# Optimization experiments

Measured on AMD Instinct MI355X. Metric: run time of the kernel, lower is better.

## Reference

```python
import jax, jax.numpy as jnp
import numpy as np

SCALE = 1.0 / 16.0      # spatial scale: image coords -> feature-map coords (stride-16 backbone)
OUT = 7                 # roi_pool_outsize
RATIO = 2               # sampling_ratio
NUM_CLASSES = 21
HID = 1024
SCORE_THRESH = 0.05
NMS_THRESH = 0.5
DET = 100               # detections_per_img
MIN_SIZE = 0.01
LOG_MAX = float(np.log(1000.0 / 16.0))  # standard bbox decode dw/dh clamp


def _bilinear(feat, ys, xs):
    # feat [C,H,W]; ys [Py], xs [Px] -> [C,Py,Px] (torchvision roi_align interpolation, aligned=False)
    C, H, W = feat.shape
    vy = (ys > -1.0) & (ys < H)
    vx = (xs > -1.0) & (xs < W)
    y = jnp.clip(ys, 0.0, H - 1.0)
    x = jnp.clip(xs, 0.0, W - 1.0)
    y0 = jnp.floor(y).astype(jnp.int32)
    x0 = jnp.floor(x).astype(jnp.int32)
    y1 = jnp.minimum(y0 + 1, H - 1)
    x1 = jnp.minimum(x0 + 1, W - 1)
    ly = (y - y0)[:, None]
    lx = (x - x0)[None, :]
    f00 = feat[:, y0[:, None], x0[None, :]]
    f01 = feat[:, y0[:, None], x1[None, :]]
    f10 = feat[:, y1[:, None], x0[None, :]]
    f11 = feat[:, y1[:, None], x1[None, :]]
    val = (f00 * (1.0 - ly) * (1.0 - lx) + f01 * (1.0 - ly) * lx
           + f10 * ly * (1.0 - lx) + f11 * ly * lx)
    return val * (vy[:, None] & vx[None, :])


def _roi_align(features, boxes, bidx):
    # features [N,C,H,W], boxes [R,4] (image coords), bidx [R] -> [R,C,OUT,OUT]
    N, C, H, W = features.shape
    b = boxes * SCALE
    rw = jnp.maximum(b[:, 2] - b[:, 0], 1.0)
    rh = jnp.maximum(b[:, 3] - b[:, 1], 1.0)
    bw = rw / OUT
    bh = rh / OUT
    # per-bin sample offsets: (ph + (i+0.5)/ratio) for ph in [0,OUT), i in [0,RATIO)
    g = (jnp.arange(OUT, dtype=jnp.float32)[:, None]
         + (jnp.arange(RATIO, dtype=jnp.float32)[None, :] + 0.5) / RATIO).reshape(-1)  # [OUT*RATIO]
    ys = b[:, 1][:, None] + g[None, :] * bh[:, None]  # [R, OUT*RATIO]
    xs = b[:, 0][:, None] + g[None, :] * bw[:, None]
    vals = jax.vmap(lambda i, yr, xr: _bilinear(features[i], yr, xr))(bidx, ys, xs)  # [R,C,P,P]
    R = boxes.shape[0]
    return vals.reshape(R, C, OUT, RATIO, OUT, RATIO).mean(axis=(3, 5))


def _decode(deltas, props):
    # deltas [R,K,4], props [R,4]; weights (10,10,5,5) as in the module
    pw = props[:, 2] - props[:, 0]
    ph = props[:, 3] - props[:, 1]
    pcx = props[:, 0] + 0.5 * pw
    pcy = props[:, 1] + 0.5 * ph
    dx = deltas[..., 0] / 10.0
    dy = deltas[..., 1] / 10.0
    dw = jnp.minimum(deltas[..., 2] / 5.0, LOG_MAX)
    dh = jnp.minimum(deltas[..., 3] / 5.0, LOG_MAX)
    cx = dx * pw[:, None] + pcx[:, None]
    cy = dy * ph[:, None] + pcy[:, None]
    w = jnp.exp(dw) * pw[:, None]
    h = jnp.exp(dh) * ph[:, None]
    return jnp.stack([cx - 0.5 * w, cy - 0.5 * h, cx + 0.5 * w, cy + 0.5 * h], axis=-1)


def _per_image(scores, boxes, img):
    # scores [S,K], boxes [S,K,4]. Drop background class, flatten, filter, class-aware NMS, top-DET.
    S, K = scores.shape
    sc = scores[:, 1:].reshape(-1)                 # [M]
    bx = boxes[:, 1:, :].reshape(-1, 4)            # [M,4]
    lb = jnp.broadcast_to(jnp.arange(1, K, dtype=jnp.int32)[None, :], (S, K - 1)).reshape(-1)
    wv = bx[:, 2] - bx[:, 0]
    hv = bx[:, 3] - bx[:, 1]
    valid = (sc > SCORE_THRESH) & (wv >= MIN_SIZE) & (hv >= MIN_SIZE)
    live0 = jnp.where(valid, sc, -1.0)
    # batched_nms via per-class coordinate offsets
    nb = bx + (lb.astype(bx.dtype) * (img + 1.0))[:, None]
    areas = (nb[:, 2] - nb[:, 0]) * (nb[:, 3] - nb[:, 1])

    def step(live, _):
        i = jnp.argmax(live)
        s = live[i]
        b = nb[i]
        xx1 = jnp.maximum(b[0], nb[:, 0])
        yy1 = jnp.maximum(b[1], nb[:, 1])
        xx2 = jnp.minimum(b[2], nb[:, 2])
        yy2 = jnp.minimum(b[3], nb[:, 3])
        inter = jnp.maximum(xx2 - xx1, 0.0) * jnp.maximum(yy2 - yy1, 0.0)
        area_i = (b[2] - b[0]) * (b[3] - b[1])
        iou = inter / (area_i + areas - inter + 1e-9)
        live = jnp.where(iou > NMS_THRESH, -1.0, live)  # also suppresses i itself (iou=1)
        return live, (i, s)

    _, (idxs, svals) = jax.lax.scan(step, live0, None, length=DET)
    keep = svals > SCORE_THRESH
    out_boxes = jnp.where(keep[:, None], bx[idxs], 0.0)
    out_scores = jnp.where(keep, svals, 0.0)
    out_labels = jnp.where(keep, lb[idxs], 0)
    return out_boxes, out_scores, out_labels


def _forward(features, proposals, w1, b1, w2, b2, wc, bc, wb, bb, image_size):
    N, C, H, W = features.shape
    S = proposals.shape[1]
    props = proposals.reshape(-1, 4)
    bidx = jnp.repeat(jnp.arange(N), S)
    feats = _roi_align(features, props, bidx)          # [R,C,7,7]
    x = feats.reshape(N * S, -1)                       # [R, C*49]
    h = jax.nn.relu(x @ w1 + b1)
    h = jax.nn.relu(h @ w2 + b2)
    cls = h @ wc + bc                                  # [R,K]
    deltas = (h @ wb + bb).reshape(N * S, NUM_CLASSES, 4)
    scores = jax.nn.softmax(cls, axis=-1)
    boxes = _decode(deltas, props)                     # [R,K,4]
    img = float(image_size)
    boxes = jnp.clip(boxes, 0.0, img)                  # square image -> clip both coords to [0,img]
    scores = scores.reshape(N, S, NUM_CLASSES)
    boxes = boxes.reshape(N, S, NUM_CLASSES, 4)
    return jax.vmap(lambda s, bx: _per_image(s, bx, img))(scores, boxes)


def setup_inputs() -> dict:
    key = jax.random.key(0)
    ks = jax.random.split(key, 12)
    N, S, C, H, W = 2, 512, 512, 50, 50
    IMG = 800
    features = jax.random.normal(ks[0], (N, C, H, W), jnp.float32)
    x1 = jax.random.uniform(ks[1], (N, S)) * (IMG - 80.0)
    y1 = jax.random.uniform(ks[2], (N, S)) * (IMG - 80.0)
    x2 = jnp.minimum(x1 + 16.0 + jax.random.uniform(ks[3], (N, S)) * 180.0, float(IMG))
    y2 = jnp.minimum(y1 + 16.0 + jax.random.uniform(ks[4], (N, S)) * 180.0, float(IMG))
    proposals = jnp.stack([x1, y1, x2, y2], axis=-1)
    D = C * OUT * OUT  # 25088
    w1 = jax.random.normal(ks[5], (D, HID), jnp.float32) * 0.01
    b1 = jnp.zeros((HID,), jnp.float32)
    w2 = jax.random.normal(ks[6], (HID, HID), jnp.float32) * 0.02
    b2 = jnp.zeros((HID,), jnp.float32)
    wc = jax.random.normal(ks[7], (HID, NUM_CLASSES), jnp.float32) * 0.05
    bc = jnp.zeros((NUM_CLASSES,), jnp.float32)
    wb = jax.random.normal(ks[8], (HID, NUM_CLASSES * 4), jnp.float32) * 0.02
    bb = jnp.zeros((NUM_CLASSES * 4,), jnp.float32)
    return {"features": features, "proposals": proposals, "w1": w1, "b1": b1,
            "w2": w2, "b2": b2, "wc": wc, "bc": bc, "wb": wb, "bb": bb,
            "image_size": IMG}


def reference(features, proposals, w1, b1, w2, b2, wc, bc, wb, bb, image_size):
    boxes, scores, labels = _forward(features, proposals, w1, b1, w2, b2, wc, bc, wb, bb, image_size)
    return boxes, scores, labels
```

## Files before the change

kernel.cpp:

```cpp
#include <hip/hip_runtime.h>
#include <cmath>

#define NIMG 2
#define SPROP 512
#define NROI 1024
#define CCH 512
#define FH 50
#define FW 50
#define K1 25088
#define HID 1024
#define NCLS 21
#define NDET 100
#define IMGSZ 800.0f
#define LOGMAX 4.135166556742356f
#define MCAND 10240
#define ZSPLIT 8
#define KCHUNK 3136
#define ZSPLIT2 4
#define KCHUNK2 256

typedef unsigned short u16;
typedef __attribute__((ext_vector_type(8))) short short8;
typedef __attribute__((ext_vector_type(4))) float f32x4;
typedef __attribute__((ext_vector_type(16))) float f32x16;

__device__ __forceinline__ u16 f2bf(float x) {
  unsigned int u = __float_as_uint(x);
  u += 0x7fffu + ((u >> 16) & 1u);
  return (u16)(u >> 16);
}
__device__ __forceinline__ float bf2f(u16 h) {
  return __uint_as_float(((unsigned int)h) << 16);
}

template <bool BF16OUT>
__global__ __launch_bounds__(256) void roi_kernel(
    const float* __restrict__ feat, const float* __restrict__ props,
    float* __restrict__ X, u16* __restrict__ Xhi, u16* __restrict__ Xlo) {
  const int r = blockIdx.x;
  const int n = r >> 9;
  const int tid = threadIdx.x;
  __shared__ float tile[32][256];
  __shared__ int sy0[14], sy1[14], sx0[14], sx1[14];
  __shared__ float sly[14], slx[14], svy[14], svx[14];

  const float p0 = props[r * 4 + 0] * 0.0625f;
  const float p1 = props[r * 4 + 1] * 0.0625f;
  const float p2 = props[r * 4 + 2] * 0.0625f;
  const float p3 = props[r * 4 + 3] * 0.0625f;
  const float bw = fmaxf(p2 - p0, 1.0f) / 7.0f;
  const float bh = fmaxf(p3 - p1, 1.0f) / 7.0f;

  if (tid < 14) {
    const int j = tid;
    const float g = (float)(j >> 1) + ((float)(j & 1) + 0.5f) * 0.5f;
    float y = p1 + g * bh;
    svy[j] = (y > -1.0f && y < (float)FH) ? 1.0f : 0.0f;
    float yc = fminf(fmaxf(y, 0.0f), (float)(FH - 1));
    int y0 = (int)floorf(yc);
    sy0[j] = y0; sy1[j] = min(y0 + 1, FH - 1); sly[j] = yc - (float)y0;
    float x = p0 + g * bw;
    svx[j] = (x > -1.0f && x < (float)FW) ? 1.0f : 0.0f;
    float xc = fminf(fmaxf(x, 0.0f), (float)(FW - 1));
    int x0 = (int)floorf(xc);
    sx0[j] = x0; sx1[j] = min(x0 + 1, FW - 1); slx[j] = xc - (float)x0;
  }
  __syncthreads();
  const int ymin = sy0[0], xmin = sx0[0];
  const float* fb = feat + (size_t)n * CCH * (FH * FW);

  for (int cc = 0; cc < 16; ++cc) {
    const int c0 = cc * 32;
#pragma unroll
    for (int e = 0; e < 32; ++e) {
      const int idx = tid + e * 256;
      const int c = idx >> 8, p = idx & 255;
      const int gy = min(ymin + (p >> 4), FH - 1);
      const int gx = min(xmin + (p & 15), FW - 1);
      tile[c][p] = fb[(size_t)(c0 + c) * (FH * FW) + gy * FW + gx];
    }
    __syncthreads();
#pragma unroll
    for (int e = 0; e < 7; ++e) {
      const int idx = tid + e * 256;
      if (idx < 1568) {
        const int c = idx / 49;
        const int s = idx - c * 49;
        const int oy = s / 7, ox = s - (s / 7) * 7;
        float acc = 0.0f;
#pragma unroll
        for (int sy = 0; sy < 2; ++sy) {
          const int yj = oy * 2 + sy;
          const int py0 = sy0[yj] - ymin, py1 = sy1[yj] - ymin;
          const float ly = sly[yj], vy = svy[yj];
#pragma unroll
          for (int sx = 0; sx < 2; ++sx) {
            const int xj = ox * 2 + sx;
            const int px0 = sx0[xj] - xmin, px1 = sx1[xj] - xmin;
            const float lx = slx[xj], vx = svx[xj];
            const float f00 = tile[c][py0 * 16 + px0];
            const float f01 = tile[c][py0 * 16 + px1];
            const float f10 = tile[c][py1 * 16 + px0];
            const float f11 = tile[c][py1 * 16 + px1];
            float v = f00 * (1.0f - ly) * (1.0f - lx) + f01 * (1.0f - ly) * lx +
                      f10 * ly * (1.0f - lx) + f11 * ly * lx;
            acc += v * (vy * vx);
          }
        }
        const float v = acc * 0.25f;
        const size_t k = (size_t)r * K1 + (size_t)(c0 + c) * 49 + s;
        if (BF16OUT) {
          const u16 h = f2bf(v);
          Xhi[k] = h;
          Xlo[k] = f2bf(v - bf2f(h));
        } else {
          X[k] = v;
        }
      }
    }
    __syncthreads();
  }
}

template <int KDIM>
__global__ __launch_bounds__(256) void convw_kernel(
    const float* __restrict__ w, u16* __restrict__ Wh, u16* __restrict__ Wl) {
  __shared__ u16 sh[64][65], sl[64][65];
  const int k0 = blockIdx.x * 64;
  const int n0 = blockIdx.y * 64;
  const int t = threadIdx.x;
#pragma unroll
  for (int e = 0; e < 16; ++e) {
    const int idx = t + e * 256;
    const int kl = idx >> 6, nl = idx & 63;
    const float v = w[(size_t)(k0 + kl) * HID + n0 + nl];
    const u16 h = f2bf(v);
    sh[kl][nl] = h;
    sl[kl][nl] = f2bf(v - bf2f(h));
  }
  __syncthreads();
#pragma unroll
  for (int e = 0; e < 16; ++e) {
    const int idx = t + e * 256;
    const int nl = idx >> 6, kl = idx & 63;
    Wh[(size_t)(n0 + nl) * KDIM + k0 + kl] = sh[kl][nl];
    Wl[(size_t)(n0 + nl) * KDIM + k0 + kl] = sl[kl][nl];
  }
}

template <int KS, int KCH>
__global__ __launch_bounds__(256, 2) void gemm_mfma_split(
    const u16* __restrict__ Ahg, const u16* __restrict__ Alg,
    const u16* __restrict__ Bhg, const u16* __restrict__ Blg,
    float* __restrict__ CP) {
  __shared__ u16 Ah[128][40], Al[128][40], Bh[128][40], Bl[128][40];
  const int tid = threadIdx.x;
  const int lane = tid & 63;
  const int wv = tid >> 6;
  const int wm = (wv >> 1) * 64;
  const int wn = (wv & 1) * 64;
  const int mT = blockIdx.y << 7;
  const int nT = blockIdx.x << 7;
  const int kz = blockIdx.z * KCH;

  const int r0 = tid >> 2, q0 = (tid & 3) << 3;
  const int r1 = r0 + 64;

  f32x16 acc[2][2];
#pragma unroll
  for (int i = 0; i < 2; ++i)
#pragma unroll
    for (int j = 0; j < 2; ++j)
#pragma unroll
      for (int e = 0; e < 16; ++e) acc[i][j][e] = 0.0f;

  const size_t a0off = (size_t)(mT + r0) * KS + q0;
  const size_t a1off = (size_t)(mT + r1) * KS + q0;
  const size_t b0off = (size_t)(nT + r0) * KS + q0;
  const size_t b1off = (size_t)(nT + r1) * KS + q0;

  const int fm = lane & 31;
  const int fq = (lane >> 5) << 3;

  uint4 va0 = *(const uint4*)(Ahg + a0off + kz);
  uint4 va1 = *(const uint4*)(Ahg + a1off + kz);
  uint4 vl0 = *(const uint4*)(Alg + a0off + kz);
  uint4 vl1 = *(const uint4*)(Alg + a1off + kz);
  uint4 vb0 = *(const uint4*)(Bhg + b0off + kz);
  uint4 vb1 = *(const uint4*)(Bhg + b1off + kz);
  uint4 vm0 = *(const uint4*)(Blg + b0off + kz);
  uint4 vm1 = *(const uint4*)(Blg + b1off + kz);

  for (int kb = kz; kb < kz + KCH; kb += 32) {
    *(uint4*)(&Ah[r0][q0]) = va0;
    *(uint4*)(&Ah[r1][q0]) = va1;
    *(uint4*)(&Al[r0][q0]) = vl0;
    *(uint4*)(&Al[r1][q0]) = vl1;
    *(uint4*)(&Bh[r0][q0]) = vb0;
    *(uint4*)(&Bh[r1][q0]) = vb1;
    *(uint4*)(&Bl[r0][q0]) = vm0;
    *(uint4*)(&Bl[r1][q0]) = vm1;
    __syncthreads();

    const int kn = kb + 32;
    if (kn < kz + KCH) {
      va0 = *(const uint4*)(Ahg + a0off + kn);
      va1 = *(const uint4*)(Ahg + a1off + kn);
      vl0 = *(const uint4*)(Alg + a0off + kn);
      vl1 = *(const uint4*)(Alg + a1off + kn);
      vb0 = *(const uint4*)(Bhg + b0off + kn);
      vb1 = *(const uint4*)(Bhg + b1off + kn);
      vm0 = *(const uint4*)(Blg + b0off + kn);
      vm1 = *(const uint4*)(Blg + b1off + kn);
    }

#pragma unroll
    for (int kh = 0; kh < 2; ++kh) {
      const int ko = kh * 16 + fq;
      short8 fah[2], fal[2], fbh[2], fbl[2];
#pragma unroll
      for (int t = 0; t < 2; ++t) {
        fah[t] = *(const short8*)(&Ah[wm + t * 32 + fm][ko]);
        fal[t] = *(const short8*)(&Al[wm + t * 32 + fm][ko]);
        fbh[t] = *(const short8*)(&Bh[wn + t * 32 + fm][ko]);
        fbl[t] = *(const short8*)(&Bl[wn + t * 32 + fm][ko]);
      }
#pragma unroll
      for (int ti = 0; ti < 2; ++ti)
#pragma unroll
        for (int tj = 0; tj < 2; ++tj) {
          acc[ti][tj] = __builtin_amdgcn_mfma_f32_32x32x16_bf16(
              fah[ti], fbh[tj], acc[ti][tj], 0, 0, 0);
          acc[ti][tj] = __builtin_amdgcn_mfma_f32_32x32x16_bf16(
              fah[ti], fbl[tj], acc[ti][tj], 0, 0, 0);
          acc[ti][tj] = __builtin_amdgcn_mfma_f32_32x32x16_bf16(
              fal[ti], fbh[tj], acc[ti][tj], 0, 0, 0);
        }
    }
    __syncthreads();
  }

  float* Cp = CP + (size_t)blockIdx.z * ((size_t)NROI * HID);
  const int ccol = nT + wn + (lane & 31);
  const int rbase = mT + wm + 4 * (lane >> 5);
#pragma unroll
  for (int ti = 0; ti < 2; ++ti)
#pragma unroll
    for (int tj = 0; tj < 2; ++tj)
#pragma unroll
      for (int rg = 0; rg < 16; ++rg) {
        const int row = rbase + ti * 32 + (rg & 3) + 8 * (rg >> 2);
        Cp[(size_t)row * HID + ccol + tj * 32] = acc[ti][tj][rg];
      }
}

__global__ __launch_bounds__(256) void gemm1_kernel(
    const float* __restrict__ A, const float* __restrict__ B,
    float* __restrict__ CP) {
  __shared__ float As[16][68];
  __shared__ float Bs[16][68];
  const int tid = threadIdx.x;
  const int mTile = blockIdx.y << 6;
  const int nTile = blockIdx.x << 6;
  const int k0 = blockIdx.z * KCHUNK;
  const int ty = tid >> 4, tx = tid & 15;
  const int ar = tid >> 2, ac = (tid & 3) << 2;
  const int br = tid >> 4, bcl = (tid & 15) << 2;
  float acc[4][4] = {};

  for (int kb = k0; kb < k0 + KCHUNK; kb += 16) {
    const float4 av = *(const float4*)(A + (size_t)(mTile + ar) * K1 + kb + ac);
    const float4 bv = *(const float4*)(B + (size_t)(kb + br) * HID + nTile + bcl);
    As[ac + 0][ar] = av.x; As[ac + 1][ar] = av.y;
    As[ac + 2][ar] = av.z; As[ac + 3][ar] = av.w;
    *(float4*)(&Bs[br][bcl]) = bv;
    __syncthreads();
#pragma unroll
    for (int kk = 0; kk < 16; ++kk) {
      const float4 a4 = *(const float4*)(&As[kk][ty << 2]);
      const float4 b4 = *(const float4*)(&Bs[kk][tx << 2]);
      const float aa[4] = {a4.x, a4.y, a4.z, a4.w};
      const float bb4[4] = {b4.x, b4.y, b4.z, b4.w};
#pragma unroll
      for (int i = 0; i < 4; ++i)
#pragma unroll
        for (int j = 0; j < 4; ++j)
          acc[i][j] = fmaf(aa[i], bb4[j], acc[i][j]);
    }
    __syncthreads();
  }
  float* Cp = CP + (size_t)blockIdx.z * (HID * NROI);
#pragma unroll
  for (int i = 0; i < 4; ++i) {
    *(float4*)(Cp + (size_t)(mTile + (ty << 2) + i) * HID + nTile + (tx << 2)) =
        make_float4(acc[i][0], acc[i][1], acc[i][2], acc[i][3]);
  }
}

__global__ __launch_bounds__(256) void bias_relu_bf16_kernel(
    const float* __restrict__ CP, const float* __restrict__ b1,
    u16* __restrict__ H1h, u16* __restrict__ H1l) {
  const int idx = blockIdx.x * 256 + threadIdx.x;
  float v = b1[idx & (HID - 1)];
#pragma unroll
  for (int z = 0; z < ZSPLIT; ++z) v += CP[(size_t)z * (HID * NROI) + idx];
  v = fmaxf(v, 0.0f);
  const u16 h = f2bf(v);
  H1h[idx] = h;
  H1l[idx] = f2bf(v - bf2f(h));
}

__global__ __launch_bounds__(256) void bias_relu_f32_kernel(
    const float* __restrict__ CP, const float* __restrict__ b1,
    float* __restrict__ H1) {
  const int idx = blockIdx.x * 256 + threadIdx.x;
  float v = b1[idx & (HID - 1)];
#pragma unroll
  for (int z = 0; z < ZSPLIT; ++z) v += CP[(size_t)z * (HID * NROI) + idx];
  H1[idx] = fmaxf(v, 0.0f);
}

__global__ __launch_bounds__(256) void bias_relu2_kernel(
    const float* __restrict__ CP2, const float* __restrict__ b2,
    float* __restrict__ H2) {
  const int idx = blockIdx.x * 256 + threadIdx.x;
  float v = b2[idx & (HID - 1)];
#pragma unroll
  for (int z = 0; z < ZSPLIT2; ++z) v += CP2[(size_t)z * (HID * NROI) + idx];
  H2[idx] = fmaxf(v, 0.0f);
}

__global__ __launch_bounds__(256) void gemm2_kernel(
    const float* __restrict__ A, const float* __restrict__ B,
    const float* __restrict__ bias, float* __restrict__ C) {
  __shared__ float As[16][68];
  __shared__ float Bs[16][68];
  const int tid = threadIdx.x;
  const int mTile = blockIdx.y << 6;
  const int nTile = blockIdx.x << 6;
  const int ty = tid >> 4, tx = tid & 15;
  const int ar = tid >> 2, ac = (tid & 3) << 2;
  const int br = tid >> 4, bcl = (tid & 15) << 2;
  float acc[4][4] = {};

  for (int kb = 0; kb < HID; kb += 16) {
    const float4 av = *(const float4*)(A + (size_t)(mTile + ar) * HID + kb + ac);
    const float4 bv = *(const float4*)(B + (size_t)(kb + br) * HID + nTile + bcl);
    As[ac + 0][ar] = av.x; As[ac + 1][ar] = av.y;
    As[ac + 2][ar] = av.z; As[ac + 3][ar] = av.w;
    *(float4*)(&Bs[br][bcl]) = bv;
    __syncthreads();
#pragma unroll
    for (int kk = 0; kk < 16; ++kk) {
      const float4 a4 = *(const float4*)(&As[kk][ty << 2]);
      const float4 b4 = *(const float4*)(&Bs[kk][tx << 2]);
      const float aa[4] = {a4.x, a4.y, a4.z, a4.w};
      const float bb4[4] = {b4.x, b4.y, b4.z, b4.w};
#pragma unroll
      for (int i = 0; i < 4; ++i)
#pragma unroll
        for (int j = 0; j < 4; ++j)
          acc[i][j] = fmaf(aa[i], bb4[j], acc[i][j]);
    }
    __syncthreads();
  }
#pragma unroll
  for (int i = 0; i < 4; ++i) {
#pragma unroll
    for (int j = 0; j < 4; ++j) {
      float v = acc[i][j] + bias[nTile + (tx << 2) + j];
      acc[i][j] = fmaxf(v, 0.0f);
    }
    *(float4*)(C + (size_t)(mTile + (ty << 2) + i) * HID + nTile + (tx << 2)) =
        make_float4(acc[i][0], acc[i][1], acc[i][2], acc[i][3]);
  }
}

__global__ __launch_bounds__(128) void heads_kernel(
    const float* __restrict__ H2m, const float* __restrict__ wc,
    const float* __restrict__ bc, const float* __restrict__ wb,
    const float* __restrict__ bb, const float* __restrict__ props,
    float* __restrict__ BX2, float* __restrict__ NB2,
    float* __restrict__ LV2) {
  const int r = blockIdx.x;
  const int tid = threadIdx.x;
  __shared__ float hrow[HID];
  __shared__ float vals[112];
  __shared__ float red[2];

  for (int i = tid; i < HID; i += 128) hrow[i] = H2m[(size_t)r * HID + i];
  __syncthreads();

  if (tid < 105) {
    float acc;
    if (tid < NCLS) {
      acc = bc[tid];
      for (int kk = 0; kk < HID; ++kk) acc = fmaf(hrow[kk], wc[kk * NCLS + tid], acc);
    } else {
      const int j = tid - NCLS;
      acc = bb[j];
      for (int kk = 0; kk < HID; ++kk) acc = fmaf(hrow[kk], wb[kk * (NCLS * 4) + j], acc);
    }
    vals[tid] = acc;
  }
  __syncthreads();

  if (tid == 0) {
    float m = vals[0];
    for (int k = 1; k < NCLS; ++k) m = fmaxf(m, vals[k]);
    float s = 0.0f;
    for (int k = 0; k < NCLS; ++k) s += expf(vals[k] - m);
    red[0] = m;
    red[1] = 1.0f / s;
  }
  __syncthreads();

  if (tid >= 1 && tid <= 20) {
    const int k = tid;
    const float prob = expf(vals[k] - red[0]) * red[1];

    const float px1 = props[r * 4 + 0], py1 = props[r * 4 + 1];
    const float px2 = props[r * 4 + 2], py2 = props[r * 4 + 3];
    const float pw = px2 - px1, ph = py2 - py1;
    const float pcx = px1 + 0.5f * pw, pcy = py1 + 0.5f * ph;

    const float dx = vals[NCLS + k * 4 + 0] / 10.0f;
    const float dy = vals[NCLS + k * 4 + 1] / 10.0f;
    const float dw = fminf(vals[NCLS + k * 4 + 2] / 5.0f, LOGMAX);
    const float dh = fminf(vals[NCLS + k * 4 + 3] / 5.0f, LOGMAX);

    const float cx = dx * pw + pcx, cy = dy * ph + pcy;
    const float w = expf(dw) * pw, h = expf(dh) * ph;
    float b0 = cx - 0.5f * w, b1c = cy - 0.5f * h;
    float b2 = cx + 0.5f * w, b3 = cy + 0.5f * h;
    b0 = fminf(fmaxf(b0, 0.0f), IMGSZ);
    b1c = fminf(fmaxf(b1c, 0.0f), IMGSZ);
    b2 = fminf(fmaxf(b2, 0.0f), IMGSZ);
    b3 = fminf(fmaxf(b3, 0.0f), IMGSZ);

    const float wv = b2 - b0, hv = b3 - b1c;
    const bool valid = (prob > 0.05f) && (wv >= 0.01f) && (hv >= 0.01f);

    const int n = r >> 9, s = r & 511;
    const int cand = (k - 1) * SPROP + s;
    const size_t bi = (size_t)n * MCAND + cand;
    const float off = (float)k * (IMGSZ + 1.0f);

    BX2[bi * 4 + 0] = b0; BX2[bi * 4 + 1] = b1c;
    BX2[bi * 4 + 2] = b2; BX2[bi * 4 + 3] = b3;
    NB2[bi * 4 + 0] = b0 + off; NB2[bi * 4 + 1] = b1c + off;
    NB2[bi * 4 + 2] = b2 + off; NB2[bi * 4 + 3] = b3 + off;
    LV2[bi] = valid ? prob : -1.0f;
  }
}

template <int CTRL>
__device__ __forceinline__ void red2(float& v, int& ix) {
  const float tv = __int_as_float(__builtin_amdgcn_update_dpp(
      (int)0xC0000000, __float_as_int(v), CTRL, 0xf, 0xf, false));
  const int ti = __builtin_amdgcn_update_dpp(0x7fffffff, ix, CTRL, 0xf, 0xf, false);
  if (tv > v || (tv == v && ti < ix)) { v = tv; ix = ti; }
}
__device__ __forceinline__ void wave_red2(float& v, int& ix) {
  red2<0x111>(v, ix);
  red2<0x112>(v, ix);
  red2<0x114>(v, ix);
  red2<0x118>(v, ix);
  red2<0x142>(v, ix);
  red2<0x143>(v, ix);
}

__global__ __launch_bounds__(64) void nms_class_kernel(
    const float* __restrict__ NB2, const float* __restrict__ LV2,
    float* __restrict__ ksg, int* __restrict__ kig, int* __restrict__ cntg) {
  const int bid = blockIdx.x;
  const int lane = threadIdx.x;
  __shared__ float4 lbox[SPROP];
  const size_t cb = (size_t)bid * SPROP;

  float lv[8], b0[8], b1[8], b2[8], b3[8], ar[8];
#pragma unroll
  for (int j = 0; j < 8; ++j) {
    const int s = lane + j * 64;
    lv[j] = LV2[cb + s];
    const float4 b = *(const float4*)(NB2 + (cb + s) * 4);
    b0[j] = b.x; b1[j] = b.y; b2[j] = b.z; b3[j] = b.w;
    ar[j] = (b.z - b.x) * (b.w - b.y);
    lbox[s] = b;
  }

  int cnt = 0;
  for (int d = 0; d < NDET; ++d) {
    float bv = -2.0f;
    int bix = 0x7fffffff;
#pragma unroll
    for (int j = 0; j < 8; ++j) {
      if (lv[j] > bv) { bv = lv[j]; bix = lane + j * 64; }
    }
    wave_red2(bv, bix);
    const float bv2 = __shfl(bv, 63);
    const int bix2 = __shfl(bix, 63);
    if (bv2 <= 0.05f) break;

    if (lane == 0) {
      ksg[bid * NDET + cnt] = bv2;
      kig[bid * NDET + cnt] = bix2;
    }
    ++cnt;

    const float4 wb = lbox[bix2];
    const float wa = (wb.z - wb.x) * (wb.w - wb.y);
#pragma unroll
    for (int j = 0; j < 8; ++j) {
      const float xx1 = fmaxf(wb.x, b0[j]);
      const float yy1 = fmaxf(wb.y, b1[j]);
      const float xx2 = fminf(wb.z, b2[j]);
      const float yy2 = fminf(wb.w, b3[j]);
      const float inter = fmaxf(xx2 - xx1, 0.0f) * fmaxf(yy2 - yy1, 0.0f);
      const float iou = inter / (wa + ar[j] - inter + 1e-9f);
      if (iou > 0.5f) lv[j] = -1.0f;
    }
  }
  if (lane == 0) cntg[bid] = cnt;
}

__global__ __launch_bounds__(1024) void nms_merge_kernel(
    const float* __restrict__ ksg, const int* __restrict__ kig,
    const int* __restrict__ cntg, const float* __restrict__ BX2,
    float* __restrict__ out) {
  const int n = blockIdx.x;
  const int tid = threadIdx.x;
  __shared__ int cbase[21];
  __shared__ unsigned long long keys[2000];
  __shared__ float ssc[2000];
  __shared__ int sfl[2000];
  __shared__ float svals[NDET];
  __shared__ int sflat[NDET];

  if (tid == 0) {
    int acc = 0;
    for (int c = 0; c < 20; ++c) { cbase[c] = acc; acc += cntg[n * 20 + c]; }
    cbase[20] = acc;
  }
  __syncthreads();
  const int T = cbase[20];

  for (int idx = tid; idx < 20 * NDET; idx += 1024) {
    const int c = idx / NDET, e = idx - (idx / NDET) * NDET;
    if (e < cntg[n * 20 + c]) {
      const int pos = cbase[c] + e;
      const float s = ksg[(n * 20 + c) * NDET + e];
      const int slot = kig[(n * 20 + c) * NDET + e];
      const int flat = slot * 20 + c;
      ssc[pos] = s;
      sfl[pos] = flat;
      keys[pos] = ((unsigned long long)__float_as_uint(s) << 32) |
                  (unsigned long long)(0xFFFFFFFFu - (unsigned)flat);
    }
  }
  __syncthreads();

  float msc[2]; int mfl[2]; unsigned long long mk[2]; int rank[2] = {0, 0};
  bool own[2];
#pragma unroll
  for (int e = 0; e < 2; ++e) {
    const int i = tid + e * 1024;
    own[e] = (i < T);
    if (own[e]) { mk[e] = keys[i]; msc[e] = ssc[i]; mfl[e] = sfl[i]; }
  }
  for (int i = 0; i < T; ++i) {
    const unsigned long long k = keys[i];
    if (own[0] && k > mk[0]) ++rank[0];
    if (own[1] && k > mk[1]) ++rank[1];
  }
#pragma unroll
  for (int e = 0; e < 2; ++e)
    if (own[e] && rank[e] < NDET) { svals[rank[e]] = msc[e]; sflat[rank[e]] = mfl[e]; }
  __syncthreads();

  if (tid < NDET) {
    const int m = (T < NDET) ? T : NDET;
    const bool keep = tid < m;
    float sv = 0.0f;
    float4 bx4 = make_float4(0.0f, 0.0f, 0.0f, 0.0f);
    float label = 0.0f;
    if (keep) {
      sv = svals[tid];
      const int flat = sflat[tid];
      const int c = flat % 20, s = flat / 20;
      bx4 = *(const float4*)(BX2 + ((size_t)(n * 20 + c) * SPROP + s) * 4);
      label = (float)(c + 1);
    }
    out[(n * NDET + tid) * 4 + 0] = bx4.x;
    out[(n * NDET + tid) * 4 + 1] = bx4.y;
    out[(n * NDET + tid) * 4 + 2] = bx4.z;
    out[(n * NDET + tid) * 4 + 3] = bx4.w;
    out[NIMG * NDET * 4 + n * NDET + tid] = sv;
    out[NIMG * NDET * 4 + NIMG * NDET + n * NDET + tid] = label;
  }
}

extern "C" void kernel_launch(void* const* d_in, const int* in_sizes, int n_in,
                              void* d_out, int out_size, void* d_ws, size_t ws_size,
                              hipStream_t stream) {
  const float* features  = (const float*)d_in[0];
  const float* proposals = (const float*)d_in[1];
  const float* w1 = (const float*)d_in[2];
  const float* b1 = (const float*)d_in[3];
  const float* w2 = (const float*)d_in[4];
  const float* b2 = (const float*)d_in[5];
  const float* wc = (const float*)d_in[6];
  const float* bc = (const float*)d_in[7];
  const float* wb = (const float*)d_in[8];
  const float* bb = (const float*)d_in[9];

  const size_t XE = (size_t)NROI * K1;
  const size_t WE = (size_t)K1 * HID;
  const size_t FLOATS_TAIL =
      (size_t)ZSPLIT * NROI * HID + 2 * (size_t)NROI * HID + (size_t)NIMG * MCAND * 10;
  const size_t NEED = (XE * 2 + WE * 2) * sizeof(u16) + FLOATS_TAIL * sizeof(float);

  if (ws_size >= NEED) {
    u16* Xhi = (u16*)d_ws;
    u16* Xlo = Xhi + XE;
    u16* Wh  = Xlo + XE;
    u16* Wl  = Wh + WE;
    float* CP  = (float*)(Wl + WE);
    float* CP2 = CP;
    float* H2  = CP + (size_t)ZSPLIT * NROI * HID;
    float* BX2 = H2 + (size_t)NROI * HID;
    float* NB2 = BX2 + (size_t)NIMG * MCAND * 4;
    float* LV2 = NB2 + (size_t)NIMG * MCAND * 4;
    float* ksg = LV2 + (size_t)NIMG * MCAND;
    int*   kig = (int*)(ksg + (size_t)NIMG * 20 * NDET);
    int*   cntg = kig + (size_t)NIMG * 20 * NDET;
    u16* H1h = Xhi;
    u16* H1l = Xhi + (size_t)NROI * HID;
    u16* W2h = Xlo;
    u16* W2l = Xlo + (size_t)HID * HID;

    convw_kernel<K1><<<dim3(K1 / 64, HID / 64), 256, 0, stream>>>(w1, Wh, Wl);
    roi_kernel<true><<<NROI, 256, 0, stream>>>(features, proposals, nullptr, Xhi, Xlo);
    gemm_mfma_split<K1, KCHUNK><<<dim3(8, 8, ZSPLIT), 256, 0, stream>>>(
        Xhi, Xlo, Wh, Wl, CP);
    bias_relu_bf16_kernel<<<(NROI * HID) / 256, 256, 0, stream>>>(CP, b1, H1h, H1l);
    convw_kernel<HID><<<dim3(HID / 64, HID / 64), 256, 0, stream>>>(w2, W2h, W2l);
    gemm_mfma_split<HID, KCHUNK2><<<dim3(8, 8, ZSPLIT2), 256, 0, stream>>>(
        H1h, H1l, W2h, W2l, CP2);
    bias_relu2_kernel<<<(NROI * HID) / 256, 256, 0, stream>>>(CP2, b2, H2);
    heads_kernel<<<NROI, 128, 0, stream>>>(H2, wc, bc, wb, bb, proposals,
                                           BX2, NB2, LV2);
    nms_class_kernel<<<NIMG * 20, 64, 0, stream>>>(NB2, LV2, ksg, kig, cntg);
    nms_merge_kernel<<<NIMG, 1024, 0, stream>>>(ksg, kig, cntg, BX2,
                                                (float*)d_out);
  } else {
    float* ws = (float*)d_ws;
    float* X   = ws;
    float* CP  = X + XE;
    float* H1  = CP + (size_t)ZSPLIT * NROI * HID;
    float* H2  = H1 + (size_t)NROI * HID;
    float* BX2 = H2 + (size_t)NROI * HID;
    float* NB2 = BX2 + (size_t)NIMG * MCAND * 4;
    float* LV2 = NB2 + (size_t)NIMG * MCAND * 4;
    float* ksg = LV2 + (size_t)NIMG * MCAND;
    int*   kig = (int*)(ksg + (size_t)NIMG * 20 * NDET);
    int*   cntg = kig + (size_t)NIMG * 20 * NDET;

    roi_kernel<false><<<NROI, 256, 0, stream>>>(features, proposals, X, nullptr, nullptr);
    gemm1_kernel<<<dim3(16, 16, ZSPLIT), 256, 0, stream>>>(X, w1, CP);
    bias_relu_f32_kernel<<<(NROI * HID) / 256, 256, 0, stream>>>(CP, b1, H1);
    gemm2_kernel<<<dim3(16, 16), 256, 0, stream>>>(H1, w2, b2, H2);
    heads_kernel<<<NROI, 128, 0, stream>>>(H2, wc, bc, wb, bb, proposals,
                                           BX2, NB2, LV2);
    nms_class_kernel<<<NIMG * 20, 64, 0, stream>>>(NB2, LV2, ksg, kig, cntg);
    nms_merge_kernel<<<NIMG, 1024, 0, stream>>>(ksg, kig, cntg, BX2,
                                                (float*)d_out);
  }
}
```

Baseline: 835.7 us.

## Restructure split-K MFMA GEMM: 512 threads, XOR-swizzled LDS, double-register prefetch, block swizzle

The split-K bf16x3 MFMA GEMM now runs 512-thread blocks of 8 waves, each wave owning a 32x64 output tile instead of 64x64. This halves per-wave accumulators so more waves fit per CU. The padded LDS tiles become unpadded 32-wide tiles with an XOR column swizzle to avoid bank conflicts. Two register stages of global loads are kept in flight across the k-loop. The first GEMM also remaps block indices so the k-split index varies fastest, to improve L2 reuse of A and B tiles. The cost is more LDS traffic per MFMA, since each wave reloads B fragments for a smaller M tile, plus extra wrap-around loads at the end of each chunk.

```diff
diff --git a/kernel.cpp b/kernel.cpp
--- a/kernel.cpp
+++ b/kernel.cpp
@@ -148,110 +148,113 @@
   }
 }
 
-template <int KS, int KCH>
-__global__ __launch_bounds__(256, 2) void gemm_mfma_split(
+template <int KS, int KCH, bool SWZ>
+__global__ __launch_bounds__(512, 4) void gemm_mfma_split(
     const u16* __restrict__ Ahg, const u16* __restrict__ Alg,
     const u16* __restrict__ Bhg, const u16* __restrict__ Blg,
     float* __restrict__ CP) {
-  __shared__ u16 Ah[128][40], Al[128][40], Bh[128][40], Bl[128][40];
+  __shared__ u16 Ah[128][32], Al[128][32], Bh[128][32], Bl[128][32];
   const int tid = threadIdx.x;
   const int lane = tid & 63;
   const int wv = tid >> 6;
-  const int wm = (wv >> 1) * 64;
-  const int wn = (wv & 1) * 64;
-  const int mT = blockIdx.y << 7;
-  const int nT = blockIdx.x << 7;
-  const int kz = blockIdx.z * KCH;
-
-  const int r0 = tid >> 2, q0 = (tid & 3) << 3;
-  const int r1 = r0 + 64;
-
-  f32x16 acc[2][2];
-#pragma unroll
-  for (int i = 0; i < 2; ++i)
-#pragma unroll
-    for (int j = 0; j < 2; ++j)
-#pragma unroll
-      for (int e = 0; e < 16; ++e) acc[i][j][e] = 0.0f;
-
-  const size_t a0off = (size_t)(mT + r0) * KS + q0;
-  const size_t a1off = (size_t)(mT + r1) * KS + q0;
-  const size_t b0off = (size_t)(nT + r0) * KS + q0;
-  const size_t b1off = (size_t)(nT + r1) * KS + q0;
+  const int wm = (wv >> 1) << 5;
+  const int wn = (wv & 1) << 6;
+
+  int bx = blockIdx.x, by = blockIdx.y, bz = blockIdx.z;
+  if (SWZ) {
+    const int f = blockIdx.x + ((blockIdx.y + (blockIdx.z << 3)) << 3);
+    bz = f & 7;
+    const int u = f >> 3;
+    bx = u & 7;
+    by = u >> 3;
+  }
+  const int mT = by << 7;
+  const int nT = bx << 7;
+  const int kz = bz * KCH;
+  const int kend = kz + KCH;
+
+  const int sr = tid >> 2;
+  const int sq = (tid & 3) << 3;
+  const int scw = (((tid & 3) ^ ((sr >> 1) & 3)) << 3);
+  const size_t aoff = (size_t)(mT + sr) * KS;
+  const size_t boff = (size_t)(nT + sr) * KS;
+
+  f32x16 acc[2];
+#pragma unroll
+  for (int j = 0; j < 2; ++j)
+#pragma unroll
+    for (int e = 0; e < 16; ++e) acc[j][e] = 0.0f;
 
   const int fm = lane & 31;
-  const int fq = (lane >> 5) << 3;
-
-  uint4 va0 = *(const uint4*)(Ahg + a0off + kz);
-  uint4 va1 = *(const uint4*)(Ahg + a1off + kz);
-  uint4 vl0 = *(const uint4*)(Alg + a0off + kz);
-  uint4 vl1 = *(const uint4*)(Alg + a1off + kz);
-  uint4 vb0 = *(const uint4*)(Bhg + b0off + kz);
-  uint4 vb1 = *(const uint4*)(Bhg + b1off + kz);
-  uint4 vm0 = *(const uint4*)(Blg + b0off + kz);
-  uint4 vm1 = *(const uint4*)(Blg + b1off + kz);
-
-  for (int kb = kz; kb < kz + KCH; kb += 32) {
-    *(uint4*)(&Ah[r0][q0]) = va0;
-    *(uint4*)(&Ah[r1][q0]) = va1;
-    *(uint4*)(&Al[r0][q0]) = vl0;
-    *(uint4*)(&Al[r1][q0]) = vl1;
-    *(uint4*)(&Bh[r0][q0]) = vb0;
-    *(uint4*)(&Bh[r1][q0]) = vb1;
-    *(uint4*)(&Bl[r0][q0]) = vm0;
-    *(uint4*)(&Bl[r1][q0]) = vm1;
-    __syncthreads();
-
-    const int kn = kb + 32;
-    if (kn < kz + KCH) {
-      va0 = *(const uint4*)(Ahg + a0off + kn);
-      va1 = *(const uint4*)(Ahg + a1off + kn);
-      vl0 = *(const uint4*)(Alg + a0off + kn);
-      vl1 = *(const uint4*)(Alg + a1off + kn);
-      vb0 = *(const uint4*)(Bhg + b0off + kn);
-      vb1 = *(const uint4*)(Bhg + b1off + kn);
-      vm0 = *(const uint4*)(Blg + b0off + kn);
-      vm1 = *(const uint4*)(Blg + b1off + kn);
-    }
-
+  const int fh = lane >> 5;
+  const int vswz = (fm >> 1) & 3;
+
+  uint4 rA = *(const uint4*)(Ahg + aoff + kz + sq);
+  uint4 rL = *(const uint4*)(Alg + aoff + kz + sq);
+  uint4 rB = *(const uint4*)(Bhg + boff + kz + sq);
+  uint4 rM = *(const uint4*)(Blg + boff + kz + sq);
+  uint4 sA = *(const uint4*)(Ahg + aoff + kz + 32 + sq);
+  uint4 sL = *(const uint4*)(Alg + aoff + kz + 32 + sq);
+  uint4 sB = *(const uint4*)(Bhg + boff + kz + 32 + sq);
+  uint4 sM = *(const uint4*)(Blg + boff + kz + 32 + sq);
+
+  auto compute = [&]() {
 #pragma unroll
     for (int kh = 0; kh < 2; ++kh) {
-      const int ko = kh * 16 + fq;
-      short8 fah[2], fal[2], fbh[2], fbl[2];
-#pragma unroll
-      for (int t = 0; t < 2; ++t) {
-        fah[t] = *(const short8*)(&Ah[wm + t * 32 + fm][ko]);
-        fal[t] = *(const short8*)(&Al[wm + t * 32 + fm][ko]);
-        fbh[t] = *(const short8*)(&Bh[wn + t * 32 + fm][ko]);
-        fbl[t] = *(const short8*)(&Bl[wn + t * 32 + fm][ko]);
+      const int cA = ((((kh << 1) | fh) ^ vswz) << 3);
+      const short8 fah = *(const short8*)(&Ah[wm + fm][cA]);
+      const short8 fal = *(const short8*)(&Al[wm + fm][cA]);
+      short8 fbh[2], fbl[2];
+      fbh[0] = *(const short8*)(&Bh[wn + fm][cA]);
+      fbh[1] = *(const short8*)(&Bh[wn + 32 + fm][cA]);
+      fbl[0] = *(const short8*)(&Bl[wn + fm][cA]);
+      fbl[1] = *(const short8*)(&Bl[wn + 32 + fm][cA]);
+#pragma unroll
+      for (int tj = 0; tj < 2; ++tj) {
+        acc[tj] = __builtin_amdgcn_mfma_f32_32x32x16_bf16(fah, fbh[tj], acc[tj], 0, 0, 0);
+        acc[tj] = __builtin_amdgcn_mfma_f32_32x32x16_bf16(fah, fbl[tj], acc[tj], 0, 0, 0);
+        acc[tj] = __builtin_amdgcn_mfma_f32_32x32x16_bf16(fal, fbh[tj], acc[tj], 0, 0, 0);
       }
-#pragma unroll
-      for (int ti = 0; ti < 2; ++ti)
-#pragma unroll
-        for (int tj = 0; tj < 2; ++tj) {
-          acc[ti][tj] = __builtin_amdgcn_mfma_f32_32x32x16_bf16(
-              fah[ti], fbh[tj], acc[ti][tj], 0, 0, 0);
-          acc[ti][tj] = __builtin_amdgcn_mfma_f32_32x32x16_bf16(
-              fah[ti], fbl[tj], acc[ti][tj], 0, 0, 0);
-          acc[ti][tj] = __builtin_amdgcn_mfma_f32_32x32x16_bf16(
-              fal[ti], fbh[tj], acc[ti][tj], 0, 0, 0);
-        }
-    }
-    __syncthreads();
-  }
-
-  float* Cp = CP + (size_t)blockIdx.z * ((size_t)NROI * HID);
-  const int ccol = nT + wn + (lane & 31);
-  const int rbase = mT + wm + 4 * (lane >> 5);
-#pragma unroll
-  for (int ti = 0; ti < 2; ++ti)
-#pragma unroll
-    for (int tj = 0; tj < 2; ++tj)
-#pragma unroll
-      for (int rg = 0; rg < 16; ++rg) {
-        const int row = rbase + ti * 32 + (rg & 3) + 8 * (rg >> 2);
-        Cp[(size_t)row * HID + ccol + tj * 32] = acc[ti][tj][rg];
-      }
+    }
+  };
+
+  for (int kb = kz; kb < kend; kb += 64) {
+    *(uint4*)(&Ah[sr][scw]) = rA;
+    *(uint4*)(&Al[sr][scw]) = rL;
+    *(uint4*)(&Bh[sr][scw]) = rB;
+    *(uint4*)(&Bl[sr][scw]) = rM;
+    __syncthreads();
+    const int kn1 = (kb + 64 < kend) ? kb + 64 : kz;
+    rA = *(const uint4*)(Ahg + aoff + kn1 + sq);
+    rL = *(const uint4*)(Alg + aoff + kn1 + sq);
+    rB = *(const uint4*)(Bhg + boff + kn1 + sq);
+    rM = *(const uint4*)(Blg + boff + kn1 + sq);
+    compute();
+    __syncthreads();
+    *(uint4*)(&Ah[sr][scw]) = sA;
+    *(uint4*)(&Al[sr][scw]) = sL;
+    *(uint4*)(&Bh[sr][scw]) = sB;
+    *(uint4*)(&Bl[sr][scw]) = sM;
+    __syncthreads();
+    const int kn2 = (kb + 96 < kend) ? kb + 96 : kz;
+    sA = *(const uint4*)(Ahg + aoff + kn2 + sq);
+    sL = *(const uint4*)(Alg + aoff + kn2 + sq);
+    sB = *(const uint4*)(Bhg + boff + kn2 + sq);
+    sM = *(const uint4*)(Blg + boff + kn2 + sq);
+    compute();
+    __syncthreads();
+  }
+
+  float* Cp = CP + (size_t)bz * ((size_t)NROI * HID);
+  const int ccol = nT + wn + fm;
+  const int rbase = mT + wm + (fh << 2);
+#pragma unroll
+  for (int tj = 0; tj < 2; ++tj)
+#pragma unroll
+    for (int rg = 0; rg < 16; ++rg) {
+      const int row = rbase + (rg & 3) + 8 * (rg >> 2);
+      Cp[(size_t)row * HID + ccol + tj * 32] = acc[tj][rg];
+    }
 }
 
 __global__ __launch_bounds__(256) void gemm1_kernel(
@@ -641,11 +644,11 @@
 
     convw_kernel<K1><<<dim3(K1 / 64, HID / 64), 256, 0, stream>>>(w1, Wh, Wl);
     roi_kernel<true><<<NROI, 256, 0, stream>>>(features, proposals, nullptr, Xhi, Xlo);
-    gemm_mfma_split<K1, KCHUNK><<<dim3(8, 8, ZSPLIT), 256, 0, stream>>>(
+    gemm_mfma_split<K1, KCHUNK, true><<<dim3(8, 8, ZSPLIT), 512, 0, stream>>>(
         Xhi, Xlo, Wh, Wl, CP);
     bias_relu_bf16_kernel<<<(NROI * HID) / 256, 256, 0, stream>>>(CP, b1, H1h, H1l);
     convw_kernel<HID><<<dim3(HID / 64, HID / 64), 256, 0, stream>>>(w2, W2h, W2l);
-    gemm_mfma_split<HID, KCHUNK2><<<dim3(8, 8, ZSPLIT2), 256, 0, stream>>>(
+    gemm_mfma_split<HID, KCHUNK2, false><<<dim3(8, 8, ZSPLIT2), 512, 0, stream>>>(
         H1h, H1l, W2h, W2l, CP2);
     bias_relu2_kernel<<<(NROI * HID) / 256, 256, 0, stream>>>(CP2, b2, H2);
     heads_kernel<<<NROI, 128, 0, stream>>>(H2, wc, bc, wb, bb, proposals,
```

Result: no change. 840.6 us (+0.6%).
